# Kernel tuning notes

Hardware: AMD Instinct MI355X
Metric: run time of the kernel (lower is better)

Reference implementation:

```python
import jax, jax.numpy as jnp
import numpy as np

N_NODES = 100000
N_EDGES = 1600000
IN_CH = 64
OUT_CH = 64
NUM_K = 9  # (degree+1)^dim = 3*3 quadratic B-spline taps; equals prod(kernel_size) here


def _quad_basis(v):
    # torch_spline_conv quadratic basis for k_mod in {0,1,2}; v = frac(pseudo*(K-deg)) = pseudo here
    return jnp.stack([0.5 * v * v - v + 0.5,
                      -v * v + v + 0.5,
                      0.5 * v * v], axis=-1)  # [E,3]


def spline_conv(x, src, dst, pseudo, W, root, bias, n_nodes):
    # W: [9, C_in, C_out]; basis B: [E, 9]
    b0 = _quad_basis(pseudo[:, 0])          # [E,3]
    b1 = _quad_basis(pseudo[:, 1])          # [E,3]
    B = (b0[:, :, None] * b1[:, None, :]).reshape(pseudo.shape[0], NUM_K)  # [E,9]
    x_src = x[src]                           # gather [E, C_in]
    msg = B[:, 0:1] * (x_src @ W[0])
    for k in range(1, NUM_K):                # fixed small loop over kernel taps
        msg = msg + B[:, k:k + 1] * (x_src @ W[k])
    out = jax.ops.segment_sum(msg, dst, num_segments=n_nodes)  # scatter-add at targets
    return out + x @ root + bias


def setup_inputs() -> dict:
    key = jax.random.key(0)
    ks = jax.random.split(key, 10)
    x = jax.random.normal(ks[0], (N_NODES, IN_CH), dtype=jnp.float32)
    edge_index = jax.random.randint(ks[1], (2, N_EDGES), 0, N_NODES, dtype=jnp.int64)
    pseudo = jax.random.uniform(ks[2], (N_EDGES, 2), dtype=jnp.float32)
    s1 = 1.0 / np.sqrt(IN_CH * NUM_K)
    s2 = 1.0 / np.sqrt(OUT_CH * NUM_K)
    W1 = jax.random.normal(ks[3], (NUM_K, IN_CH, OUT_CH), dtype=jnp.float32) * s1
    root1 = jax.random.normal(ks[4], (IN_CH, OUT_CH), dtype=jnp.float32) * s1
    b1 = jax.random.normal(ks[5], (OUT_CH,), dtype=jnp.float32) * 0.01
    W2 = jax.random.normal(ks[6], (NUM_K, OUT_CH, OUT_CH), dtype=jnp.float32) * s2
    root2 = jax.random.normal(ks[7], (OUT_CH, OUT_CH), dtype=jnp.float32) * s2
    b2 = jax.random.normal(ks[8], (OUT_CH,), dtype=jnp.float32) * 0.01
    return {"x": x, "edge_index": edge_index, "pseudo": pseudo,
            "W1": W1, "root1": root1, "b1": b1,
            "W2": W2, "root2": root2, "b2": b2}


def reference(x, edge_index, pseudo, W1, root1, b1, W2, root2, b2):
    src, dst = edge_index[0], edge_index[1]  # PyG: aggregate messages at target
    h = jax.nn.relu(spline_conv(x, src, dst, pseudo, W1, root1, b1, N_NODES))
    h = jax.nn.relu(spline_conv(h, src, dst, pseudo, W2, root2, b2, N_NODES))
    return h
```

## Files before the change

### kernel.cpp

```cpp
#include <hip/hip_runtime.h>
#include <stdint.h>

typedef __attribute__((ext_vector_type(8))) short bf16x8;
typedef __attribute__((ext_vector_type(4))) float f32x4;

__device__ __forceinline__ float bf2f(unsigned short u) {
  union { unsigned int i; float f; } x; x.i = ((unsigned int)u) << 16; return x.f;
}
__device__ __forceinline__ unsigned short f2bf(float f) {
  union { float f; unsigned int i; } x; x.f = f;
  unsigned int i = x.i;
  return (unsigned short)((i + 0x7FFFu + ((i >> 16) & 1u)) >> 16);
}
__device__ __forceinline__ float f16lo(unsigned int u) {
  union { unsigned short s; _Float16 h; } x; x.s = (unsigned short)(u & 0xFFFFu);
  return (float)x.h;
}
__device__ __forceinline__ float f16hi(unsigned int u) {
  union { unsigned short s; _Float16 h; } x; x.s = (unsigned short)(u >> 16);
  return (float)x.h;
}
__device__ __forceinline__ unsigned int packf16(float a, float b) {
  union { unsigned short s; _Float16 h; } x, y;
  x.h = (_Float16)a; y.h = (_Float16)b;
  return (unsigned int)x.s | ((unsigned int)y.s << 16);
}


__global__ void count_kernel(const int* __restrict__ ei, int E, int* __restrict__ counts) {
  int e = blockIdx.x * blockDim.x + threadIdx.x;
  if (e < E) atomicAdd(&counts[ei[E + e]], 1);
}

__global__ void scan1_kernel(const int* __restrict__ counts, int n, int* __restrict__ bsum) {
  int i = blockIdx.x * 256 + threadIdx.x;
  int v = (i < n) ? counts[i] : 0;
  int lane = threadIdx.x & 63, w = threadIdx.x >> 6;
  for (int d = 32; d > 0; d >>= 1) v += __shfl_down(v, d, 64);
  __shared__ int ws[4];
  if (lane == 0) ws[w] = v;
  __syncthreads();
  if (threadIdx.x == 0) bsum[blockIdx.x] = ws[0] + ws[1] + ws[2] + ws[3];
}

__global__ void scan2_kernel(int* __restrict__ bsum, int G) {
  int t = threadIdx.x;
  int c = (G + 511) >> 9;
  int lo = min(t * c, G), hi = min(lo + c, G);
  int s = 0;
  for (int i = lo; i < hi; ++i) s += bsum[i];
  int lane = t & 63, w = t >> 6;
  int incl = s;
  for (int d = 1; d < 64; d <<= 1) { int u = __shfl_up(incl, d, 64); if (lane >= d) incl += u; }
  __shared__ int wsum[8];
  if (lane == 63) wsum[w] = incl;
  __syncthreads();
  int wpre = 0;
  for (int i = 0; i < w; ++i) wpre += wsum[i];
  int excl = wpre + incl - s;
  for (int i = lo; i < hi; ++i) { int v = bsum[i]; bsum[i] = excl; excl += v; }
}

__global__ void scan3_kernel(const int* __restrict__ counts, int n, const int* __restrict__ bsum,
                             int* __restrict__ offsets, int* __restrict__ cursor, int total) {
  int i = blockIdx.x * 256 + threadIdx.x;
  int v = (i < n) ? counts[i] : 0;
  int lane = threadIdx.x & 63, w = threadIdx.x >> 6;
  int incl = v;
  for (int d = 1; d < 64; d <<= 1) { int u = __shfl_up(incl, d, 64); if (lane >= d) incl += u; }
  __shared__ int wsum[4];
  if (lane == 63) wsum[w] = incl;
  __syncthreads();
  int pre = bsum[blockIdx.x];
  for (int j = 0; j < w; ++j) pre += wsum[j];
  if (i < n) {
    int excl = pre + incl - v;
    offsets[i] = excl;
    cursor[i] = excl;
  }
  if (i == 0) offsets[n] = total;
}


__global__ void fill_kernel(const int* __restrict__ ei, const float* __restrict__ pseudo,
                            int E, int* __restrict__ cursor, uint4* __restrict__ recs) {
  int e = blockIdx.x * blockDim.x + threadIdx.x;
  if (e >= E) return;
  int d = ei[E + e];
  int s = ei[e];
  float2 uv = ((const float2*)pseudo)[e];
  float u = uv.x, v = uv.y;
  float b0 = 0.5f * u * u - u + 0.5f, b1 = -u * u + u + 0.5f, b2 = 0.5f * u * u;
  float c0 = 0.5f * v * v - v + 0.5f, c1 = -v * v + v + 0.5f, c2 = 0.5f * v * v;
  int p = atomicAdd(&cursor[d], 1);
  uint4 r;
  r.x = ((unsigned int)s) << 7;
  r.y = packf16(b0, b1);
  r.z = packf16(b2, c0);
  r.w = packf16(c1, c2);
  recs[p] = r;
}


__global__ void wconv_kernel(const float* __restrict__ W, const float* __restrict__ root,
                             unsigned short* __restrict__ Wt) {
  int i = blockIdx.x * blockDim.x + threadIdx.x;
  if (i >= 640 * 64) return;
  int co = i / 640, r = i % 640;
  float v = (r < 576) ? W[r * 64 + co] : root[(r - 576) * 64 + co];
  Wt[i] = f2bf(v);
}


__global__ void xconv_kernel(const float4* __restrict__ x4, ushort4* __restrict__ xh4, int n4) {
  int i = blockIdx.x * blockDim.x + threadIdx.x;
  if (i < n4) {
    float4 v = x4[i];
    ushort4 o;
    o.x = f2bf(v.x); o.y = f2bf(v.y); o.z = f2bf(v.z); o.w = f2bf(v.w);
    xh4[i] = o;
  }
}


#define SROW 648
#define RECCAP 384

#define UNPACK_FMA(RY, RZ, RW, XV)                                 \
  {                                                                \
    float b0 = f16lo(RY), b1 = f16hi(RY), b2 = f16lo(RZ);          \
    float c0 = f16hi(RZ), c1 = f16lo(RW), c2 = f16hi(RW);          \
    float t0 = b0 * (XV), t1 = b1 * (XV), t2 = b2 * (XV);          \
    a0 += t0 * c0; a1 += t0 * c1; a2 += t0 * c2;                   \
    a3 += t1 * c0; a4 += t1 * c1; a5 += t1 * c2;                   \
    a6 += t2 * c0; a7 += t2 * c1; a8 += t2 * c2;                   \
  }

#define AGG_LOOP(RECEXPR)                                                       \
  {                                                                             \
    int m = end - beg;                                                          \
    int j = 0;                                                                  \
    for (; j + 8 <= m; j += 8) {                                                \
      uint4 R[8];                                                               \
      _Pragma("unroll") for (int k = 0; k < 8; ++k) R[k] = RECEXPR(j + k);      \
      float xv[8];                                                              \
      _Pragma("unroll") for (int k = 0; k < 8; ++k)                             \
          xv[k] = bf2f(*(const unsigned short*)(Xb + R[k].x + laneB));          \
      _Pragma("unroll") for (int k = 0; k < 8; ++k)                             \
          UNPACK_FMA(R[k].y, R[k].z, R[k].w, xv[k]);                            \
    }                                                                           \
    for (; j < m; ++j) {                                                        \
      uint4 r = RECEXPR(j);                                                     \
      float xv = bf2f(*(const unsigned short*)(Xb + r.x + laneB));              \
      UNPACK_FMA(r.y, r.z, r.w, xv);                                            \
    }                                                                           \
  }

template <bool OUTBF16>
__global__ __launch_bounds__(512) void fused_kernel(const int* __restrict__ offsets,
                                                    const uint4* __restrict__ recs,
                                                    const unsigned short* __restrict__ Xh,
                                                    const unsigned short* __restrict__ Wt,
                                                    const float* __restrict__ bias,
                                                    void* __restrict__ outv, int N) {
  __shared__ short sA[16 * SROW];
  __shared__ uint4 sRec[RECCAP];
  int tid = threadIdx.x, w = tid >> 6, lane = tid & 63;
  int nodeBase = blockIdx.x * 16;
  int nTop = min(nodeBase + 16, N);
  const char* Xb = (const char*)Xh;
  unsigned int laneB = (unsigned int)lane * 2u;

  int blockBeg = offsets[nodeBase];
  int stage = min(offsets[nTop] - blockBeg, RECCAP);
  for (int i = tid; i < stage; i += 512) sRec[i] = recs[(size_t)blockBeg + i];
  __syncthreads();

#pragma unroll
  for (int t = 0; t < 2; ++t) {
    int row = w * 2 + t;
    int n = nodeBase + row;
    if (n < N) {
      int beg = __builtin_amdgcn_readfirstlane(offsets[n]);
      int end = __builtin_amdgcn_readfirstlane(offsets[n + 1]);
      float a0 = 0.f, a1 = 0.f, a2 = 0.f, a3 = 0.f, a4 = 0.f,
            a5 = 0.f, a6 = 0.f, a7 = 0.f, a8 = 0.f;
      int lbeg = beg - blockBeg;
      if (end - blockBeg <= RECCAP) {
#define RECL(i) sRec[lbeg + (i)]
        AGG_LOOP(RECL)
#undef RECL
      } else {
#define RECG(i) recs[(size_t)beg + (i)]
        AGG_LOOP(RECG)
#undef RECG
      }
      float self = bf2f(Xh[(size_t)n * 64 + lane]);
      int rb = row * SROW;
      sA[rb + 0 * 64 + lane] = (short)f2bf(a0);
      sA[rb + 1 * 64 + lane] = (short)f2bf(a1);
      sA[rb + 2 * 64 + lane] = (short)f2bf(a2);
      sA[rb + 3 * 64 + lane] = (short)f2bf(a3);
      sA[rb + 4 * 64 + lane] = (short)f2bf(a4);
      sA[rb + 5 * 64 + lane] = (short)f2bf(a5);
      sA[rb + 6 * 64 + lane] = (short)f2bf(a6);
      sA[rb + 7 * 64 + lane] = (short)f2bf(a7);
      sA[rb + 8 * 64 + lane] = (short)f2bf(a8);
      sA[rb + 576 + lane] = (short)f2bf(self);
    }
  }
  __syncthreads();

  if (w < 4) {
    int r15 = lane & 15, kg = lane >> 4;
    f32x4 acc = {0.f, 0.f, 0.f, 0.f};
#pragma unroll
    for (int kk = 0; kk < 20; ++kk) {
      int kbase = kk * 32 + kg * 8;
      bf16x8 af = *(const bf16x8*)(&sA[r15 * SROW + kbase]);
      bf16x8 bfr = *(const bf16x8*)(Wt + (size_t)(w * 16 + r15) * 640 + kbase);
      acc = __builtin_amdgcn_mfma_f32_16x16x32_bf16(af, bfr, acc, 0, 0, 0);
    }
    int col = w * 16 + r15;
    float bv = bias[col];
    int row0 = kg * 4;
#pragma unroll
    for (int r = 0; r < 4; ++r) {
      int node = nodeBase + row0 + r;
      if (node < N) {
        float val = fmaxf(acc[r] + bv, 0.f);
        size_t idx = (size_t)node * 64 + col;
        if (OUTBF16) ((unsigned short*)outv)[idx] = f2bf(val);
        else ((float*)outv)[idx] = val;
      }
    }
  }
}


extern "C" void kernel_launch(void* const* d_in, const int* in_sizes, int n_in,
                              void* d_out, int out_size, void* d_ws, size_t ws_size,
                              hipStream_t stream) {
  const float* x = (const float*)d_in[0];
  const int* ei = (const int*)d_in[1];
  const float* pseudo = (const float*)d_in[2];
  const float* W1 = (const float*)d_in[3];
  const float* root1 = (const float*)d_in[4];
  const float* b1 = (const float*)d_in[5];
  const float* W2 = (const float*)d_in[6];
  const float* root2 = (const float*)d_in[7];
  const float* b2 = (const float*)d_in[8];

  const int N = in_sizes[0] / 64;
  const int E = in_sizes[1] / 2;
  const int G = (N + 255) / 256;

  char* p = (char*)d_ws;
  auto carve = [&](size_t bytes) -> void* {
    void* r = (void*)p;
    p += (bytes + 255) & ~(size_t)255;
    return r;
  };
  int* counts = (int*)carve((size_t)N * 4);
  int* offsets = (int*)carve((size_t)(N + 1) * 4);
  int* cursor = (int*)carve((size_t)N * 4);
  int* bsum = (int*)carve((size_t)G * 4);
  uint4* recs = (uint4*)carve((size_t)E * 16);
  unsigned short* Wt1 = (unsigned short*)carve(640 * 64 * 2);
  unsigned short* Wt2 = (unsigned short*)carve(640 * 64 * 2);
  unsigned short* h = (unsigned short*)carve((size_t)N * 64 * 2);
  unsigned short* xh = (unsigned short*)carve((size_t)N * 64 * 2);
  (void)ws_size;

  hipMemsetAsync(counts, 0, (size_t)N * 4, stream);
  count_kernel<<<(E + 255) / 256, 256, 0, stream>>>(ei, E, counts);
  scan1_kernel<<<G, 256, 0, stream>>>(counts, N, bsum);
  scan2_kernel<<<1, 512, 0, stream>>>(bsum, G);
  scan3_kernel<<<G, 256, 0, stream>>>(counts, N, bsum, offsets, cursor, E);
  fill_kernel<<<(E + 255) / 256, 256, 0, stream>>>(ei, pseudo, E, cursor, recs);
  wconv_kernel<<<160, 256, 0, stream>>>(W1, root1, Wt1);
  wconv_kernel<<<160, 256, 0, stream>>>(W2, root2, Wt2);
  xconv_kernel<<<(N * 16 + 255) / 256, 256, 0, stream>>>((const float4*)x, (ushort4*)xh, N * 16);

  int FB = (N + 15) / 16;
  fused_kernel<true><<<FB, 512, 0, stream>>>(offsets, recs, xh, Wt1, b1, (void*)h, N);
  fused_kernel<false><<<FB, 512, 0, stream>>>(offsets, recs, h, Wt2, b2, d_out, N);
}
```

Measured before the change: 524.8 us.

## Stage gathered source rows into LDS cooperatively before per-node aggregation

Before aggregating, the whole block cooperatively gathers the neighbour feature rows into shared memory using 16-byte vector loads, with 8 threads per 128-byte row. The per-wave aggregation loop then reads both records and features from LDS, pads its unrolled tail with zeroed weights, and falls back to global loads for records past the cap. This replaces scattered 2-byte per-lane global gathers with coalesced wide loads, adding an extra barrier. It uses about 37KB more LDS, which may reduce occupancy, and the staging cap drops from 384 to 288 records.

```diff
diff --git a/kernel.cpp b/kernel.cpp
--- a/kernel.cpp
+++ b/kernel.cpp
@@ -124,7 +124,7 @@
 
 
 #define SROW 648
-#define RECCAP 384
+#define CAP 288
 
 #define UNPACK_FMA(RY, RZ, RW, XV)                                 \
   {                                                                \
@@ -136,26 +136,6 @@
     a6 += t2 * c0; a7 += t2 * c1; a8 += t2 * c2;                   \
   }
 
-#define AGG_LOOP(RECEXPR)                                                       \
-  {                                                                             \
-    int m = end - beg;                                                          \
-    int j = 0;                                                                  \
-    for (; j + 8 <= m; j += 8) {                                                \
-      uint4 R[8];                                                               \
-      _Pragma("unroll") for (int k = 0; k < 8; ++k) R[k] = RECEXPR(j + k);      \
-      float xv[8];                                                              \
-      _Pragma("unroll") for (int k = 0; k < 8; ++k)                             \
-          xv[k] = bf2f(*(const unsigned short*)(Xb + R[k].x + laneB));          \
-      _Pragma("unroll") for (int k = 0; k < 8; ++k)                             \
-          UNPACK_FMA(R[k].y, R[k].z, R[k].w, xv[k]);                            \
-    }                                                                           \
-    for (; j < m; ++j) {                                                        \
-      uint4 r = RECEXPR(j);                                                     \
-      float xv = bf2f(*(const unsigned short*)(Xb + r.x + laneB));              \
-      UNPACK_FMA(r.y, r.z, r.w, xv);                                            \
-    }                                                                           \
-  }
-
 template <bool OUTBF16>
 __global__ __launch_bounds__(512) void fused_kernel(const int* __restrict__ offsets,
                                                     const uint4* __restrict__ recs,
@@ -163,8 +143,9 @@
                                                     const unsigned short* __restrict__ Wt,
                                                     const float* __restrict__ bias,
                                                     void* __restrict__ outv, int N) {
-  __shared__ short sA[16 * SROW];
-  __shared__ uint4 sRec[RECCAP];
+  __shared__ __align__(16) short sA[16 * SROW];
+  __shared__ __align__(16) uint4 sRec[CAP];
+  __shared__ __align__(16) unsigned short sXg[CAP * 64];
   int tid = threadIdx.x, w = tid >> 6, lane = tid & 63;
   int nodeBase = blockIdx.x * 16;
   int nTop = min(nodeBase + 16, N);
@@ -172,8 +153,23 @@
   unsigned int laneB = (unsigned int)lane * 2u;
 
   int blockBeg = offsets[nodeBase];
-  int stage = min(offsets[nTop] - blockBeg, RECCAP);
+  int blockEnd = offsets[nTop];
+  int stage = min(blockEnd - blockBeg, CAP);
+
   for (int i = tid; i < stage; i += 512) sRec[i] = recs[(size_t)blockBeg + i];
+  __syncthreads();
+  {
+    int chunk = tid & 7;
+    int rbase = tid >> 3;
+    for (int r0 = 0; r0 < stage; r0 += 64) {
+      int r = r0 + rbase;
+      if (r < stage) {
+        unsigned int so = sRec[r].x;
+        uint4 v = *(const uint4*)(Xb + so + chunk * 16);
+        *(uint4*)((char*)sXg + r * 128 + chunk * 16) = v;
+      }
+    }
+  }
   __syncthreads();
 
 #pragma unroll
@@ -183,19 +179,29 @@
     if (n < N) {
       int beg = __builtin_amdgcn_readfirstlane(offsets[n]);
       int end = __builtin_amdgcn_readfirstlane(offsets[n + 1]);
+      unsigned short selfu = Xh[(size_t)n * 64 + lane];
       float a0 = 0.f, a1 = 0.f, a2 = 0.f, a3 = 0.f, a4 = 0.f,
             a5 = 0.f, a6 = 0.f, a7 = 0.f, a8 = 0.f;
       int lbeg = beg - blockBeg;
-      if (end - blockBeg <= RECCAP) {
-#define RECL(i) sRec[lbeg + (i)]
-        AGG_LOOP(RECL)
-#undef RECL
-      } else {
-#define RECG(i) recs[(size_t)beg + (i)]
-        AGG_LOOP(RECG)
-#undef RECG
-      }
-      float self = bf2f(Xh[(size_t)n * 64 + lane]);
+      int lend = end - blockBeg;
+      int lcap = min(lend, CAP);
+      int m = lcap - lbeg;
+      for (int j0 = 0; j0 < m; j0 += 4) {
+#pragma unroll
+        for (int k = 0; k < 4; ++k) {
+          int idx = j0 + k;
+          int le = lbeg + (idx < m ? idx : 0);
+          uint4 r = sRec[le];
+          float xv = bf2f(sXg[le * 64 + lane]);
+          if (idx >= m) { r.y = 0u; r.z = 0u; r.w = 0u; }
+          UNPACK_FMA(r.y, r.z, r.w, xv)
+        }
+      }
+      for (int j = (lbeg > lcap ? lbeg : lcap); j < lend; ++j) {
+        uint4 r = recs[(size_t)blockBeg + j];
+        float xv = bf2f(*(const unsigned short*)(Xb + r.x + laneB));
+        UNPACK_FMA(r.y, r.z, r.w, xv)
+      }
       int rb = row * SROW;
       sA[rb + 0 * 64 + lane] = (short)f2bf(a0);
       sA[rb + 1 * 64 + lane] = (short)f2bf(a1);
@@ -206,7 +212,7 @@
       sA[rb + 6 * 64 + lane] = (short)f2bf(a6);
       sA[rb + 7 * 64 + lane] = (short)f2bf(a7);
       sA[rb + 8 * 64 + lane] = (short)f2bf(a8);
-      sA[rb + 576 + lane] = (short)f2bf(self);
+      sA[rb + 576 + lane] = (short)selfu;
     }
   }
   __syncthreads();
```

Result: no change. 520.8 us (-0.8%).
